# Kernel optimization log

Hardware: AMD Instinct MI355X
Metric: run time of the kernel (lower is better)

The kernel has to match this reference:

```python
import jax, jax.numpy as jnp
import numpy as np

N_Q_HEADS = 32
N_KV_HEADS = 8
GROUP = N_Q_HEADS // N_KV_HEADS  # 4


def _rope(x, cos, sin):
    # x: [b, s, h, d]; cos/sin: [s, d//2]. Complex rotation on (even, odd) pairs,
    # matching torch.view_as_complex on reshape(..., -1, 2).
    b, s, h, d = x.shape
    xr = x.reshape(b, s, h, d // 2, 2)
    x0, x1 = xr[..., 0], xr[..., 1]
    c = cos[None, :, None, :]
    sn = sin[None, :, None, :]
    o0 = x0 * c - x1 * sn
    o1 = x0 * sn + x1 * c
    return jnp.stack([o0, o1], axis=-1).reshape(b, s, h, d)


def setup_inputs() -> dict:
    key = jax.random.key(0)
    B, S, D = 2, 2048, 4096
    HD = D // N_Q_HEADS  # 128
    ks = jax.random.split(key, 8)
    x = jax.random.normal(ks[0], (B, S, D), jnp.float32)
    # True rotary table (theta = 10000), as cos/sin of shape [S, HD//2]
    inv_freq = 1.0 / (10000.0 ** (jnp.arange(0, HD, 2, dtype=jnp.float32) / HD))
    ang = jnp.outer(jnp.arange(S, dtype=jnp.float32), inv_freq)
    freqs_cos = jnp.cos(ang)
    freqs_sin = jnp.sin(ang)
    sc = 0.02
    qw = jax.random.normal(ks[1], (D, N_Q_HEADS * HD), jnp.float32) * sc
    qb = jax.random.normal(ks[2], (N_Q_HEADS * HD,), jnp.float32) * sc
    kw = jax.random.normal(ks[3], (D, N_KV_HEADS * HD), jnp.float32) * sc
    kb = jax.random.normal(ks[4], (N_KV_HEADS * HD,), jnp.float32) * sc
    vw = jax.random.normal(ks[5], (D, N_KV_HEADS * HD), jnp.float32) * sc
    vb = jax.random.normal(ks[6], (N_KV_HEADS * HD,), jnp.float32) * sc
    ow = jax.random.normal(ks[7], (D, D), jnp.float32) * sc
    return dict(x=x, freqs_cos=freqs_cos, freqs_sin=freqs_sin,
                qw=qw, qb=qb, kw=kw, kb=kb, vw=vw, vb=vb, ow=ow, start_pos=0)


def reference(x, freqs_cos, freqs_sin, qw, qb, kw, kb, vw, vb, ow, start_pos):
    b, s, dim = x.shape
    hd = dim // N_Q_HEADS
    q = (x @ qw + qb).reshape(b, s, N_Q_HEADS, hd)
    k = (x @ kw + kb).reshape(b, s, N_KV_HEADS, hd)
    v = (x @ vw + vb).reshape(b, s, N_KV_HEADS, hd)
    cos = freqs_cos[start_pos:start_pos + s]
    sin = freqs_sin[start_pos:start_pos + s]
    q = _rope(q, cos, sin)
    k = _rope(k, cos, sin)
    # start_pos == 0: cache write then slice is identity on fresh k/v.
    # GQA: query head h = kv_head * GROUP + g (matches torch repeat+reshape).
    q = q.transpose(0, 2, 1, 3).reshape(b, N_KV_HEADS, GROUP, s, hd)
    k = k.transpose(0, 2, 1, 3)  # [b, Hkv, s, hd]
    v = v.transpose(0, 2, 1, 3)
    scores = jnp.einsum('bhgqd,bhkd->bhgqk', q, k) / jnp.sqrt(jnp.float32(hd))
    causal = jnp.tril(jnp.ones((s, s), bool))
    scores = jnp.where(causal[None, None, None], scores, jnp.float32(-1e30))
    p = jax.nn.softmax(scores, axis=-1)
    o = jnp.einsum('bhgqk,bhkd->bhgqd', p, v)
    o = o.reshape(b, N_Q_HEADS, s, hd).transpose(0, 2, 1, 3).reshape(b, s, dim)
    return o @ ow
```

## Files before the change

kernel.cpp:

```cpp
#include <hip/hip_runtime.h>
#include <hip/hip_bf16.h>
#include <stdint.h>

typedef __bf16 bf16_t;
typedef __bf16 bf16x8 __attribute__((ext_vector_type(8)));
typedef __bf16 bf16x4 __attribute__((ext_vector_type(4)));
typedef float f32x4 __attribute__((ext_vector_type(4)));

typedef __attribute__((address_space(1))) unsigned gu32;
typedef __attribute__((address_space(3))) unsigned lu32;

__device__ __forceinline__ unsigned short f2bf(float f) {
  unsigned u = __builtin_bit_cast(unsigned, f);
  unsigned r = (u + 0x7FFFu + ((u >> 16) & 1u)) >> 16;
  return (unsigned short)r;
}

__device__ __forceinline__ void gload_lds16(const bf16_t* g, bf16_t* l) {
  __builtin_amdgcn_global_load_lds((const gu32*)(const void*)g, (lu32*)(void*)l, 16, 0, 0);
}

__global__ __launch_bounds__(256) void k_cvt_bf16(const float* __restrict__ in,
                                                  bf16_t* __restrict__ out, int n4) {
  int i = blockIdx.x * 256 + threadIdx.x;
  if (i >= n4) return;
  float4 v = ((const float4*)in)[i];
  ushort4 o;
  o.x = f2bf(v.x); o.y = f2bf(v.y); o.z = f2bf(v.z); o.w = f2bf(v.w);
  ((ushort4*)out)[i] = o;
}

__global__ __launch_bounds__(256) void k_transpose_cvt(const float* __restrict__ in,
                                                       bf16_t* __restrict__ out, int R, int C) {
  __shared__ float t[32][33];
  int c0 = blockIdx.x * 32, r0 = blockIdx.y * 32;
  int tx = threadIdx.x & 31, ty = threadIdx.x >> 5;
  #pragma unroll
  for (int r = 0; r < 4; ++r) {
    int rr = ty + r * 8;
    t[rr][tx] = in[(size_t)(r0 + rr) * C + c0 + tx];
  }
  __syncthreads();
  #pragma unroll
  for (int r = 0; r < 4; ++r) {
    int rr = ty + r * 8;
    ((unsigned short*)out)[(size_t)(c0 + rr) * R + r0 + tx] = f2bf(t[tx][rr]);
  }
}

__global__ __launch_bounds__(256) void k_transpose_bf16(const bf16_t* __restrict__ in,
                                                        bf16_t* __restrict__ out, int R, int C) {
  __shared__ unsigned short t[32][33];
  const unsigned short* ip = (const unsigned short*)in + (size_t)blockIdx.z * R * C;
  unsigned short* op = (unsigned short*)out + (size_t)blockIdx.z * R * C;
  int c0 = blockIdx.x * 32, r0 = blockIdx.y * 32;
  int tx = threadIdx.x & 31, ty = threadIdx.x >> 5;
  #pragma unroll
  for (int r = 0; r < 4; ++r) {
    int rr = ty + r * 8;
    t[rr][tx] = ip[(size_t)(r0 + rr) * C + c0 + tx];
  }
  __syncthreads();
  #pragma unroll
  for (int r = 0; r < 4; ++r) {
    int rr = ty + r * 8;
    op[(size_t)(c0 + rr) * R + r0 + tx] = t[tx][rr];
  }
}

#define BK 32
__global__ __launch_bounds__(256) void k_gemm_qkv(
    const bf16_t* __restrict__ A, const bf16_t* __restrict__ Bm,
    const float* __restrict__ qb, const float* __restrict__ kb, const float* __restrict__ vb,
    const float* __restrict__ cosT, const float* __restrict__ sinT,
    const int* __restrict__ start_pos,
    bf16_t* __restrict__ Qr, bf16_t* __restrict__ Kr, bf16_t* __restrict__ Vr) {
  __shared__ __attribute__((aligned(16))) bf16_t sA[128 * BK];
  __shared__ __attribute__((aligned(16))) bf16_t sB[128 * BK];
  __shared__ __attribute__((aligned(16))) bf16_t sET[128][132];
  const int tid = threadIdx.x;
  const int lane = tid & 63;
  const int wv = tid >> 6;
  const int wr = wv >> 1, wc = wv & 1;
  const int bid = blockIdx.y * gridDim.x + blockIdx.x;
  const int swz = (bid & 7) * 192 + (bid >> 3);
  const int brow = (swz & 31) * 128;
  const int bcol = (swz >> 5) * 128;
  const int K = 4096;
  const int l4 = lane >> 2;
  const int c8 = (lane & 3) * 8;
  const int fr = lane & 15;
  const int fq = lane >> 4;

  f32x4 acc[4][4];
  #pragma unroll
  for (int i = 0; i < 4; ++i)
    #pragma unroll
    for (int j = 0; j < 4; ++j) acc[i][j] = (f32x4){0.f, 0.f, 0.f, 0.f};

  for (int k0 = 0; k0 < K; k0 += BK) {
    #pragma unroll
    for (int r = 0; r < 2; ++r) {
      int chunk = r * 4 + wv;
      int row = chunk * 16 + l4;
      gload_lds16(A + (size_t)(brow + row) * K + k0 + c8, sA + chunk * 512);
      gload_lds16(Bm + (size_t)(bcol + row) * K + k0 + c8, sB + chunk * 512);
    }
    __syncthreads();
    bf16x8 af[4], bfv[4];
    #pragma unroll
    for (int mi = 0; mi < 4; ++mi)
      af[mi] = *(const bf16x8*)(sA + (wr * 64 + mi * 16 + fr) * BK + fq * 8);
    #pragma unroll
    for (int ni = 0; ni < 4; ++ni)
      bfv[ni] = *(const bf16x8*)(sB + (wc * 64 + ni * 16 + fr) * BK + fq * 8);
    #pragma unroll
    for (int mi = 0; mi < 4; ++mi)
      #pragma unroll
      for (int ni = 0; ni < 4; ++ni)
        acc[mi][ni] = __builtin_amdgcn_mfma_f32_16x16x32_bf16(af[mi], bfv[ni], acc[mi][ni], 0, 0, 0);
    __syncthreads();
  }

  const int sp = *start_pos;
  const bool isQ = bcol < 4096;
  const bool isV = bcol >= 5120;
  const int s0 = brow & 2047;
  #pragma unroll
  for (int mi = 0; mi < 4; ++mi) {
    #pragma unroll
    for (int ni = 0; ni < 4; ++ni) {
      int lc = wc * 64 + ni * 16 + fr;
      float bias = isQ ? qb[bcol + lc] : (!isV ? kb[bcol - 4096 + lc] : vb[bcol - 5120 + lc]);
      int lrb = wr * 64 + mi * 16 + fq * 4;
      bf16x4 pk;
      #pragma unroll
      for (int j = 0; j < 4; ++j) {
        float v = acc[mi][ni][j] + bias;
        float partner = __shfl_xor(v, 1);
        if (!isV) {
          int dd = lc >> 1;
          int s = s0 + lrb + j;
          float cc = cosT[(size_t)(sp + s) * 64 + dd];
          float sn = sinT[(size_t)(sp + s) * 64 + dd];
          v = (lc & 1) ? (partner * sn + v * cc) : (v * cc - partner * sn);
        }
        pk[j] = (bf16_t)v;
      }
      *(bf16x4*)&sET[lc][lrb] = pk;
    }
  }
  __syncthreads();
  const int b = brow >> 11;
  unsigned short* dst;
  if (isQ)
    dst = (unsigned short*)Qr + (((size_t)b * 32 + (bcol >> 7)) * 2048 + s0) * 128;
  else if (!isV)
    dst = (unsigned short*)Kr + (((size_t)b * 8 + ((bcol - 4096) >> 7)) * 2048 + s0) * 128;
  else
    dst = (unsigned short*)Vr + (((size_t)b * 8 + ((bcol - 5120) >> 7)) * 2048 + s0) * 128;
  #pragma unroll
  for (int i = 0; i < 8; ++i) {
    int chunk = i * 256 + tid;
    int sl = chunk >> 4;
    int dp = (chunk & 15) * 8;
    unsigned short tmp[8];
    #pragma unroll
    for (int k = 0; k < 8; ++k) tmp[k] = ((unsigned short*)sET)[(dp + k) * 132 + sl];
    uint4 ov;
    ov.x = (unsigned)tmp[0] | ((unsigned)tmp[1] << 16);
    ov.y = (unsigned)tmp[2] | ((unsigned)tmp[3] << 16);
    ov.z = (unsigned)tmp[4] | ((unsigned)tmp[5] << 16);
    ov.w = (unsigned)tmp[6] | ((unsigned)tmp[7] << 16);
    *(uint4*)(dst + (size_t)sl * 128 + dp) = ov;
  }
}

__global__ __launch_bounds__(256) void k_attn(
    const bf16_t* __restrict__ Qr, const bf16_t* __restrict__ Kr,
    const bf16_t* __restrict__ Vt, bf16_t* __restrict__ Ob) {
  __shared__ __attribute__((aligned(16))) bf16_t sK[2][4096];
  __shared__ __attribute__((aligned(16))) bf16_t sV[2][4096];
  __shared__ __attribute__((aligned(16))) bf16_t p_lds[4][16][40];

  const int tid = threadIdx.x;
  const int lane = tid & 63;
  const int w = tid >> 6;
  const int b = blockIdx.y >> 5, h = blockIdx.y & 31;
  const int hk = h >> 2;
  const int qt = (int)gridDim.x - 1 - (int)blockIdx.x;
  const int q0b = qt * 128;
  const int T = qt * 4 + 4;
  const bf16_t* Qb = Qr + (((size_t)b * 32 + h) * 2048) * 128;
  const bf16_t* Kb = Kr + (((size_t)b * 8 + hk) * 2048) * 128;
  const bf16_t* Vb = Vt + (((size_t)b * 8 + hk) * 128) * 2048;
  const int fr = lane & 15, fq = lane >> 4;
  const int qw0 = q0b + w * 32;
  const float sc = 0.08838834764831845f;

  const int c0 = w * 64 + lane;
  const int c1 = 256 + w * 64 + lane;
  const int krow0 = c0 >> 4, krow1 = c1 >> 4;
  const int ko0 = ((c0 & 15) << 4) ^ ((krow0 & 7) << 4);
  const int ko1 = ((c1 & 15) << 4) ^ ((krow1 & 7) << 4);
  const size_t ksrc0 = (size_t)krow0 * 128 + (ko0 >> 1);
  const size_t ksrc1 = (size_t)krow1 * 128 + (ko1 >> 1);
  const int vr0 = c0 >> 3, vr1 = c1 >> 3;
  const int vo0 = ((c0 & 7) << 4) ^ ((vr0 & 7) << 4);
  const int vo1 = ((c1 & 7) << 4) ^ ((vr1 & 7) << 4);
  const size_t vsrc0 = (size_t)(2 * vr0 + (vo0 >> 6)) * 2048 + ((vo0 & 63) >> 1);
  const size_t vsrc1 = (size_t)(2 * vr1 + (vo1 >> 6)) * 2048 + ((vo1 & 63) >> 1);
  const int ldsA = (w * 64) * 8;
  const int ldsB = (256 + w * 64) * 8;

  bf16x8 qf[2][4];
  #pragma unroll
  for (int f = 0; f < 2; ++f)
    #pragma unroll
    for (int c = 0; c < 4; ++c)
      qf[f][c] = *(const bf16x8*)(Qb + (size_t)(qw0 + f * 16 + fr) * 128 + c * 32 + fq * 8);

  f32x4 o[2][8];
  #pragma unroll
  for (int f = 0; f < 2; ++f)
    #pragma unroll
    for (int i = 0; i < 8; ++i) o[f][i] = (f32x4){0.f, 0.f, 0.f, 0.f};
  float m_s[2] = {-1e30f, -1e30f}, l_s[2] = {0.f, 0.f};

  const int kswz = (fr & 7) << 4;
  const int vlane = (fr >> 1) * 128 + ((((fr & 1) << 6) | (fq << 4)) ^ ((fr >> 1) << 4));

  auto STAGE = [&](int buf, int kv0) {
    const bf16_t* Kt = Kb + (size_t)kv0 * 128;
    const bf16_t* Vg = Vb + kv0;
    bf16_t* sk = &sK[buf][0];
    bf16_t* sv = &sV[buf][0];
    gload_lds16(Kt + ksrc0, sk + ldsA);
    gload_lds16(Kt + ksrc1, sk + ldsB);
    gload_lds16(Vg + vsrc0, sv + ldsA);
    gload_lds16(Vg + vsrc1, sv + ldsB);
  };

  STAGE(0, 0);
  int cur = 0;
  for (int t = 0; t < T; ++t) {
    const int kv0 = t * 32;
    if (t + 1 < T) {
      STAGE(cur ^ 1, kv0 + 32);
      asm volatile("s_waitcnt vmcnt(4)" ::: "memory");
    } else {
      asm volatile("s_waitcnt vmcnt(0)" ::: "memory");
    }
    __builtin_amdgcn_s_barrier();

    if (kv0 <= qw0 + 31) {
      const char* skc = (const char*)&sK[cur][0];
      const char* svc = (const char*)&sV[cur][0];
      f32x4 st[2][2];
      #pragma unroll
      for (int f = 0; f < 2; ++f)
        #pragma unroll
        for (int s2 = 0; s2 < 2; ++s2) st[f][s2] = (f32x4){0.f, 0.f, 0.f, 0.f};
      __builtin_amdgcn_s_setprio(1);
      #pragma unroll
      for (int c = 0; c < 4; ++c) {
        const int off = (((c << 6) | (fq << 4)) ^ kswz);
        bf16x8 kf0 = *(const bf16x8*)(skc + fr * 256 + off);
        bf16x8 kf1 = *(const bf16x8*)(skc + 4096 + fr * 256 + off);
        st[0][0] = __builtin_amdgcn_mfma_f32_16x16x32_bf16(kf0, qf[0][c], st[0][0], 0, 0, 0);
        st[0][1] = __builtin_amdgcn_mfma_f32_16x16x32_bf16(kf1, qf[0][c], st[0][1], 0, 0, 0);
        st[1][0] = __builtin_amdgcn_mfma_f32_16x16x32_bf16(kf0, qf[1][c], st[1][0], 0, 0, 0);
        st[1][1] = __builtin_amdgcn_mfma_f32_16x16x32_bf16(kf1, qf[1][c], st[1][1], 0, 0, 0);
      }
      __builtin_amdgcn_s_setprio(0);
      bf16x8 pa[2];
      #pragma unroll
      for (int f = 0; f < 2; ++f) {
        const int qg = qw0 + f * 16 + fr;
        float p0[4], p1[4];
        float pm = -1e30f;
        #pragma unroll
        for (int j = 0; j < 4; ++j) {
          int kvr = kv0 + fq * 4 + j;
          float s0v = (kvr <= qg) ? st[f][0][j] * sc : -1e30f;
          float s1v = (kvr + 16 <= qg) ? st[f][1][j] * sc : -1e30f;
          p0[j] = s0v; p1[j] = s1v;
          pm = fmaxf(pm, fmaxf(s0v, s1v));
        }
        pm = fmaxf(pm, __shfl_xor(pm, 16));
        pm = fmaxf(pm, __shfl_xor(pm, 32));
        if (!__all(pm <= m_s[f] + 8.0f)) {
          float m_new = fmaxf(m_s[f], pm);
          float scf = __expf(m_s[f] - m_new);
          l_s[f] *= scf;
          #pragma unroll
          for (int j = 0; j < 4; ++j) {
            float sj = __shfl(scf, fq * 4 + j);
            #pragma unroll
            for (int df = 0; df < 8; ++df) o[f][df][j] *= sj;
          }
          m_s[f] = m_new;
        }
        float ps = 0.f;
        #pragma unroll
        for (int j = 0; j < 4; ++j) {
          p0[j] = __expf(p0[j] - m_s[f]);
          p1[j] = __expf(p1[j] - m_s[f]);
          ps += p0[j] + p1[j];
        }
        ps += __shfl_xor(ps, 16);
        ps += __shfl_xor(ps, 32);
        l_s[f] += ps;
        bf16x4 pk0, pk1;
        #pragma unroll
        for (int j = 0; j < 4; ++j) { pk0[j] = (bf16_t)p0[j]; pk1[j] = (bf16_t)p1[j]; }
        *(bf16x4*)&p_lds[w][fr][fq * 4] = pk0;
        *(bf16x4*)&p_lds[w][fr][16 + fq * 4] = pk1;
        asm volatile("s_waitcnt lgkmcnt(0)" ::: "memory");
        pa[f] = *(const bf16x8*)&p_lds[w][fr][fq * 8];
        asm volatile("s_waitcnt lgkmcnt(0)" ::: "memory");
      }
      __builtin_amdgcn_s_setprio(1);
      #pragma unroll
      for (int df = 0; df < 8; ++df) {
        bf16x8 vf = *(const bf16x8*)(svc + df * 1024 + vlane);
        o[0][df] = __builtin_amdgcn_mfma_f32_16x16x32_bf16(pa[0], vf, o[0][df], 0, 0, 0);
        o[1][df] = __builtin_amdgcn_mfma_f32_16x16x32_bf16(pa[1], vf, o[1][df], 0, 0, 0);
      }
      __builtin_amdgcn_s_setprio(0);
    }
    __builtin_amdgcn_sched_barrier(0);
    __builtin_amdgcn_s_barrier();
    cur ^= 1;
  }

  #pragma unroll
  for (int f = 0; f < 2; ++f) {
    #pragma unroll
    for (int j = 0; j < 4; ++j) {
      float lj = __shfl(l_s[f], fq * 4 + j);
      float rl = 1.f / lj;
      int srow = qw0 + f * 16 + fq * 4 + j;
      #pragma unroll
      for (int df = 0; df < 8; ++df) {
        int dcol = df * 16 + fr;
        ((unsigned short*)Ob)[((size_t)b * 2048 + srow) * 4096 + h * 128 + dcol] =
            f2bf(o[f][df][j] * rl);
      }
    }
  }
}

__global__ __launch_bounds__(256) void k_gemm_out(
    const bf16_t* __restrict__ A, const bf16_t* __restrict__ Bm, float* __restrict__ out) {
  __shared__ __attribute__((aligned(16))) bf16_t sA[128 * BK];
  __shared__ __attribute__((aligned(16))) bf16_t sB[128 * BK];
  const int tid = threadIdx.x;
  const int lane = tid & 63;
  const int wv = tid >> 6;
  const int wr = wv >> 1, wc = wv & 1;
  const int bid = blockIdx.y * gridDim.x + blockIdx.x;
  const int swz = (bid & 7) * 128 + (bid >> 3);
  const int brow = (swz & 31) * 128;
  const int bcol = (swz >> 5) * 128;
  const int K = 4096;
  const int l4 = lane >> 2;
  const int c8 = (lane & 3) * 8;
  const int fr = lane & 15;
  const int fq = lane >> 4;

  f32x4 acc[4][4];
  #pragma unroll
  for (int i = 0; i < 4; ++i)
    #pragma unroll
    for (int j = 0; j < 4; ++j) acc[i][j] = (f32x4){0.f, 0.f, 0.f, 0.f};

  for (int k0 = 0; k0 < K; k0 += BK) {
    #pragma unroll
    for (int r = 0; r < 2; ++r) {
      int chunk = r * 4 + wv;
      int row = chunk * 16 + l4;
      gload_lds16(A + (size_t)(brow + row) * K + k0 + c8, sA + chunk * 512);
      gload_lds16(Bm + (size_t)(bcol + row) * K + k0 + c8, sB + chunk * 512);
    }
    __syncthreads();
    bf16x8 af[4], bfv[4];
    #pragma unroll
    for (int mi = 0; mi < 4; ++mi)
      af[mi] = *(const bf16x8*)(sA + (wr * 64 + mi * 16 + fr) * BK + fq * 8);
    #pragma unroll
    for (int ni = 0; ni < 4; ++ni)
      bfv[ni] = *(const bf16x8*)(sB + (wc * 64 + ni * 16 + fr) * BK + fq * 8);
    #pragma unroll
    for (int mi = 0; mi < 4; ++mi)
      #pragma unroll
      for (int ni = 0; ni < 4; ++ni)
        acc[mi][ni] = __builtin_amdgcn_mfma_f32_16x16x32_bf16(af[mi], bfv[ni], acc[mi][ni], 0, 0, 0);
    __syncthreads();
  }

  #pragma unroll
  for (int mi = 0; mi < 4; ++mi)
    #pragma unroll
    for (int ni = 0; ni < 4; ++ni) {
      int col = bcol + wc * 64 + ni * 16 + fr;
      #pragma unroll
      for (int j = 0; j < 4; ++j) {
        int row = brow + wr * 64 + mi * 16 + fq * 4 + j;
        out[(size_t)row * 4096 + col] = acc[mi][ni][j];
      }
    }
}

extern "C" void kernel_launch(void* const* d_in, const int* in_sizes, int n_in,
                              void* d_out, int out_size, void* d_ws, size_t ws_size,
                              hipStream_t stream) {
  const float* x    = (const float*)d_in[0];
  const float* cosT = (const float*)d_in[1];
  const float* sinT = (const float*)d_in[2];
  const float* qw   = (const float*)d_in[3];
  const float* qb   = (const float*)d_in[4];
  const float* kw   = (const float*)d_in[5];
  const float* kb   = (const float*)d_in[6];
  const float* vw   = (const float*)d_in[7];
  const float* vb   = (const float*)d_in[8];
  const float* ow   = (const float*)d_in[9];
  const int*   sp   = (const int*)d_in[10];
  float* out = (float*)d_out;
  char* ws = (char*)d_ws;

  bf16_t* xb  = (bf16_t*)(ws + 0);
  bf16_t* Ob  = (bf16_t*)(ws + 0);
  bf16_t* wT  = (bf16_t*)(ws + (size_t)33554432);
  bf16_t* owT = (bf16_t*)(ws + (size_t)83886080);
  bf16_t* Qr  = (bf16_t*)(ws + (size_t)117440512);
  bf16_t* Kr  = (bf16_t*)(ws + (size_t)150994944);
  bf16_t* Vr  = (bf16_t*)(ws + (size_t)159383552);
  bf16_t* Vt  = (bf16_t*)(ws + (size_t)167772160);

  k_cvt_bf16<<<16384, 256, 0, stream>>>(x, xb, 2 * 2048 * 4096 / 4);
  k_transpose_cvt<<<dim3(128, 128), 256, 0, stream>>>(qw, wT, 4096, 4096);
  k_transpose_cvt<<<dim3(32, 128), 256, 0, stream>>>(kw, wT + (size_t)4096 * 4096, 4096, 1024);
  k_transpose_cvt<<<dim3(32, 128), 256, 0, stream>>>(vw, wT + (size_t)5120 * 4096, 4096, 1024);
  k_transpose_cvt<<<dim3(128, 128), 256, 0, stream>>>(ow, owT, 4096, 4096);

  k_gemm_qkv<<<dim3(32, 48), 256, 0, stream>>>(xb, wT, qb, kb, vb, cosT, sinT, sp, Qr, Kr, Vr);
  k_transpose_bf16<<<dim3(4, 64, 16), 256, 0, stream>>>(Vr, Vt, 2048, 128);
  k_attn<<<dim3(16, 64), 256, 0, stream>>>(Qr, Kr, Vt, Ob);
  k_gemm_out<<<dim3(32, 32), 256, 0, stream>>>(Ob, owT, out);
}
```

Baseline: 958.7 us.

## Replace both GEMMs with a pipelined 256x256-tile, 512-thread templated kernel

Merges the QKV and output projection GEMMs into one templated kernel. It uses 256x256 block tiles, 8 waves and double-buffered 128KB dynamic LDS with XOR-swizzled layouts. Global-to-LDS loads for the next K tile are interleaved with MFMA half-steps, paced by explicit vmcnt waits, raw barriers and s_setprio around MFMA bursts. This raises data reuse per loaded byte and hides load latency, at the cost of fewer blocks per CU and a partial last wave for the QKV grid (384 blocks). The RoPE/bias epilogue is run in two passes through an LDS transpose buffer.

```diff
diff --git a/kernel.cpp b/kernel.cpp
--- a/kernel.cpp
+++ b/kernel.cpp
@@ -19,6 +19,9 @@
 __device__ __forceinline__ void gload_lds16(const bf16_t* g, bf16_t* l) {
   __builtin_amdgcn_global_load_lds((const gu32*)(const void*)g, (lu32*)(void*)l, 16, 0, 0);
 }
+
+#define BARRIER() do { asm volatile("" ::: "memory"); __builtin_amdgcn_s_barrier(); asm volatile("" ::: "memory"); } while (0)
+#define WAITV(N) asm volatile("s_waitcnt vmcnt(" #N ")" ::: "memory")
 
 __global__ __launch_bounds__(256) void k_cvt_bf16(const float* __restrict__ in,
                                                   bf16_t* __restrict__ out, int n4) {
@@ -68,111 +71,167 @@
   }
 }
 
-#define BK 32
-__global__ __launch_bounds__(256) void k_gemm_qkv(
+template <int MODE>
+__global__ __launch_bounds__(512, 2) void k_gemm256(
     const bf16_t* __restrict__ A, const bf16_t* __restrict__ Bm,
     const float* __restrict__ qb, const float* __restrict__ kb, const float* __restrict__ vb,
     const float* __restrict__ cosT, const float* __restrict__ sinT,
     const int* __restrict__ start_pos,
-    bf16_t* __restrict__ Qr, bf16_t* __restrict__ Kr, bf16_t* __restrict__ Vr) {
-  __shared__ __attribute__((aligned(16))) bf16_t sA[128 * BK];
-  __shared__ __attribute__((aligned(16))) bf16_t sB[128 * BK];
-  __shared__ __attribute__((aligned(16))) bf16_t sET[128][132];
+    bf16_t* __restrict__ Qr, bf16_t* __restrict__ Kr, bf16_t* __restrict__ Vr,
+    float* __restrict__ outF, int nbq) {
+  extern __shared__ char smem[];
+  bf16_t* sAe = (bf16_t*)smem;
+  bf16_t* sBe = (bf16_t*)(smem + 65536);
   const int tid = threadIdx.x;
   const int lane = tid & 63;
-  const int wv = tid >> 6;
-  const int wr = wv >> 1, wc = wv & 1;
-  const int bid = blockIdx.y * gridDim.x + blockIdx.x;
-  const int swz = (bid & 7) * 192 + (bid >> 3);
-  const int brow = (swz & 31) * 128;
-  const int bcol = (swz >> 5) * 128;
-  const int K = 4096;
-  const int l4 = lane >> 2;
-  const int c8 = (lane & 3) * 8;
-  const int fr = lane & 15;
-  const int fq = lane >> 4;
-
-  f32x4 acc[4][4];
-  #pragma unroll
-  for (int i = 0; i < 4; ++i)
-    #pragma unroll
-    for (int j = 0; j < 4; ++j) acc[i][j] = (f32x4){0.f, 0.f, 0.f, 0.f};
-
-  for (int k0 = 0; k0 < K; k0 += BK) {
-    #pragma unroll
-    for (int r = 0; r < 2; ++r) {
-      int chunk = r * 4 + wv;
-      int row = chunk * 16 + l4;
-      gload_lds16(A + (size_t)(brow + row) * K + k0 + c8, sA + chunk * 512);
-      gload_lds16(Bm + (size_t)(bcol + row) * K + k0 + c8, sB + chunk * 512);
+  const int w = tid >> 6;
+  const int wr = w >> 2, wc = w & 3;
+  const int fr = lane & 15, fq = lane >> 4;
+  const int g = (blockIdx.x & 7) * nbq + (blockIdx.x >> 3);
+  const int brow = (g & 15) * 256;
+  const int bcol = (g >> 4) * 256;
+
+  const int srow = w * 16 + (lane >> 2);
+  const int scol = (((lane & 3) ^ ((lane >> 3) & 3))) * 8;
+  const bf16_t* Ag = A + (size_t)(brow + srow) * 4096 + scol;
+  const bf16_t* Bg = Bm + (size_t)(bcol + srow) * 4096 + scol;
+  bf16_t* sAw = sAe + w * 512;
+  bf16_t* sBw = sBe + w * 512;
+
+  const int swz = (fr >> 1) & 3;
+  const int aoff = (wr * 128 + fr) * 32 + (fq ^ swz) * 8;
+  const int boff = (wc * 64 + fr) * 32 + (fq ^ swz) * 8;
+
+  f32x4 acc[8][4];
+  #pragma unroll
+  for (int m = 0; m < 8; ++m)
+    #pragma unroll
+    for (int n = 0; n < 4; ++n) acc[m][n] = (f32x4){0.f, 0.f, 0.f, 0.f};
+
+  auto stageA = [&](int buf, int kh, int kt) {
+    const bf16_t* gp = Ag + (size_t)kt * 64 + kh * 32;
+    bf16_t* lp = sAw + (buf * 2 + kh) * 8192;
+    gload_lds16(gp, lp);
+    gload_lds16(gp + (size_t)128 * 4096, lp + 4096);
+  };
+  auto stageB = [&](int buf, int kh, int kt) {
+    const bf16_t* gp = Bg + (size_t)kt * 64 + kh * 32;
+    bf16_t* lp = sBw + (buf * 2 + kh) * 8192;
+    gload_lds16(gp, lp);
+    gload_lds16(gp + (size_t)128 * 4096, lp + 4096);
+  };
+
+  bf16x8 afv[4], bfv[4];
+#define LOADB(BUF, KH) { const bf16_t* p = sBe + ((BUF) * 2 + (KH)) * 8192 + boff; \
+  _Pragma("unroll") for (int n = 0; n < 4; ++n) bfv[n] = *(const bf16x8*)(p + n * 512); }
+#define LOADA(BUF, KH, MH) { const bf16_t* p = sAe + ((BUF) * 2 + (KH)) * 8192 + aoff + (MH) * 2048; \
+  _Pragma("unroll") for (int m = 0; m < 4; ++m) afv[m] = *(const bf16x8*)(p + m * 512); }
+#define MFMAH(MH) do { __builtin_amdgcn_s_setprio(1); \
+  _Pragma("unroll") for (int m = 0; m < 4; ++m) \
+    _Pragma("unroll") for (int n = 0; n < 4; ++n) \
+      acc[(MH) * 4 + m][n] = __builtin_amdgcn_mfma_f32_16x16x32_bf16(afv[m], bfv[n], acc[(MH) * 4 + m][n], 0, 0, 0); \
+  __builtin_amdgcn_s_setprio(0); } while (0)
+
+  stageA(0, 0, 0); stageB(0, 0, 0);
+  stageA(0, 1, 0); stageB(0, 1, 0);
+  WAITV(4);
+  BARRIER();
+
+  for (int kt = 0; kt < 63; ++kt) {
+    const int cur = kt & 1, nxt = cur ^ 1;
+    LOADB(cur, 0); LOADA(cur, 0, 0); stageA(nxt, 0, kt + 1);
+    BARRIER(); MFMAH(0); BARRIER();
+    LOADA(cur, 0, 1); stageB(nxt, 0, kt + 1);
+    BARRIER(); MFMAH(1); WAITV(4); BARRIER();
+    LOADB(cur, 1); LOADA(cur, 1, 0); stageA(nxt, 1, kt + 1);
+    BARRIER(); MFMAH(0); BARRIER();
+    LOADA(cur, 1, 1); stageB(nxt, 1, kt + 1);
+    BARRIER(); MFMAH(1); WAITV(4); BARRIER();
+  }
+  LOADB(1, 0); LOADA(1, 0, 0); BARRIER(); MFMAH(0); BARRIER();
+  LOADA(1, 0, 1); BARRIER(); MFMAH(1); WAITV(0); BARRIER();
+  LOADB(1, 1); LOADA(1, 1, 0); BARRIER(); MFMAH(0); BARRIER();
+  LOADA(1, 1, 1); MFMAH(1);
+#undef LOADB
+#undef LOADA
+#undef MFMAH
+
+  __syncthreads();
+
+  if constexpr (MODE == 0) {
+    const int sp2 = *start_pos;
+    const int b = brow >> 11;
+    const int s0 = brow & 2047;
+    const bool isV = (bcol >= 5120);
+    unsigned short* sET = (unsigned short*)smem;
+    const int hh = wc >> 1;
+    const int dbase = (wc & 1) * 64;
+    #pragma unroll
+    for (int pass = 0; pass < 2; ++pass) {
+      if (hh == pass) {
+        #pragma unroll
+        for (int n = 0; n < 4; ++n) {
+          const int d = dbase + n * 16 + fr;
+          const int col = bcol + pass * 128 + d;
+          float bias;
+          if (bcol < 4096) bias = qb[col];
+          else if (bcol < 5120) bias = kb[col - 4096];
+          else bias = vb[col - 5120];
+          #pragma unroll
+          for (int m = 0; m < 8; ++m) {
+            const int sl = wr * 128 + m * 16 + fq * 4;
+            bf16x4 pk;
+            #pragma unroll
+            for (int j = 0; j < 4; ++j) {
+              float v = acc[m][n][j] + bias;
+              float partner = __shfl_xor(v, 1);
+              if (!isV) {
+                int s = s0 + sl + j;
+                float cc = cosT[(size_t)(sp2 + s) * 64 + (d >> 1)];
+                float sn = sinT[(size_t)(sp2 + s) * 64 + (d >> 1)];
+                v = (d & 1) ? (partner * sn + v * cc) : (v * cc - partner * sn);
+              }
+              pk[j] = (bf16_t)v;
+            }
+            *(bf16x4*)&sET[d * 268 + sl] = pk;
+          }
+        }
+      }
+      __syncthreads();
+      const int cb = bcol + pass * 128;
+      unsigned short* Hdst;
+      if (cb < 4096)      Hdst = (unsigned short*)Qr + (((size_t)b * 32 + (cb >> 7)) * 2048 + s0) * 128;
+      else if (cb < 5120) Hdst = (unsigned short*)Kr + (((size_t)b * 8 + ((cb - 4096) >> 7)) * 2048 + s0) * 128;
+      else                Hdst = (unsigned short*)Vr + (((size_t)b * 8 + ((cb - 5120) >> 7)) * 2048 + s0) * 128;
+      #pragma unroll
+      for (int i = 0; i < 8; ++i) {
+        int c = i * 512 + tid;
+        int sl = c >> 4;
+        int dp = (c & 15) * 8;
+        unsigned short tmp[8];
+        #pragma unroll
+        for (int k2 = 0; k2 < 8; ++k2) tmp[k2] = sET[(dp + k2) * 268 + sl];
+        uint4 ov;
+        ov.x = (unsigned)tmp[0] | ((unsigned)tmp[1] << 16);
+        ov.y = (unsigned)tmp[2] | ((unsigned)tmp[3] << 16);
+        ov.z = (unsigned)tmp[4] | ((unsigned)tmp[5] << 16);
+        ov.w = (unsigned)tmp[6] | ((unsigned)tmp[7] << 16);
+        *(uint4*)(Hdst + (size_t)sl * 128 + dp) = ov;
+      }
+      __syncthreads();
     }
-    __syncthreads();
-    bf16x8 af[4], bfv[4];
-    #pragma unroll
-    for (int mi = 0; mi < 4; ++mi)
-      af[mi] = *(const bf16x8*)(sA + (wr * 64 + mi * 16 + fr) * BK + fq * 8);
-    #pragma unroll
-    for (int ni = 0; ni < 4; ++ni)
-      bfv[ni] = *(const bf16x8*)(sB + (wc * 64 + ni * 16 + fr) * BK + fq * 8);
-    #pragma unroll
-    for (int mi = 0; mi < 4; ++mi)
-      #pragma unroll
-      for (int ni = 0; ni < 4; ++ni)
-        acc[mi][ni] = __builtin_amdgcn_mfma_f32_16x16x32_bf16(af[mi], bfv[ni], acc[mi][ni], 0, 0, 0);
-    __syncthreads();
-  }
-
-  const int sp = *start_pos;
-  const bool isQ = bcol < 4096;
-  const bool isV = bcol >= 5120;
-  const int s0 = brow & 2047;
-  #pragma unroll
-  for (int mi = 0; mi < 4; ++mi) {
-    #pragma unroll
-    for (int ni = 0; ni < 4; ++ni) {
-      int lc = wc * 64 + ni * 16 + fr;
-      float bias = isQ ? qb[bcol + lc] : (!isV ? kb[bcol - 4096 + lc] : vb[bcol - 5120 + lc]);
-      int lrb = wr * 64 + mi * 16 + fq * 4;
-      bf16x4 pk;
-      #pragma unroll
-      for (int j = 0; j < 4; ++j) {
-        float v = acc[mi][ni][j] + bias;
-        float partner = __shfl_xor(v, 1);
-        if (!isV) {
-          int dd = lc >> 1;
-          int s = s0 + lrb + j;
-          float cc = cosT[(size_t)(sp + s) * 64 + dd];
-          float sn = sinT[(size_t)(sp + s) * 64 + dd];
-          v = (lc & 1) ? (partner * sn + v * cc) : (v * cc - partner * sn);
+  } else {
+    #pragma unroll
+    for (int m = 0; m < 8; ++m)
+      #pragma unroll
+      for (int n = 0; n < 4; ++n) {
+        const int col = bcol + wc * 64 + n * 16 + fr;
+        #pragma unroll
+        for (int j = 0; j < 4; ++j) {
+          const int row = brow + wr * 128 + m * 16 + fq * 4 + j;
+          outF[(size_t)row * 4096 + col] = acc[m][n][j];
         }
-        pk[j] = (bf16_t)v;
-      }
-      *(bf16x4*)&sET[lc][lrb] = pk;
-    }
-  }
-  __syncthreads();
-  const int b = brow >> 11;
-  unsigned short* dst;
-  if (isQ)
-    dst = (unsigned short*)Qr + (((size_t)b * 32 + (bcol >> 7)) * 2048 + s0) * 128;
-  else if (!isV)
-    dst = (unsigned short*)Kr + (((size_t)b * 8 + ((bcol - 4096) >> 7)) * 2048 + s0) * 128;
-  else
-    dst = (unsigned short*)Vr + (((size_t)b * 8 + ((bcol - 5120) >> 7)) * 2048 + s0) * 128;
-  #pragma unroll
-  for (int i = 0; i < 8; ++i) {
-    int chunk = i * 256 + tid;
-    int sl = chunk >> 4;
-    int dp = (chunk & 15) * 8;
-    unsigned short tmp[8];
-    #pragma unroll
-    for (int k = 0; k < 8; ++k) tmp[k] = ((unsigned short*)sET)[(dp + k) * 132 + sl];
-    uint4 ov;
-    ov.x = (unsigned)tmp[0] | ((unsigned)tmp[1] << 16);
-    ov.y = (unsigned)tmp[2] | ((unsigned)tmp[3] << 16);
-    ov.z = (unsigned)tmp[4] | ((unsigned)tmp[5] << 16);
-    ov.w = (unsigned)tmp[6] | ((unsigned)tmp[7] << 16);
-    *(uint4*)(dst + (size_t)sl * 128 + dp) = ov;
+      }
   }
 }
 
@@ -351,67 +410,6 @@
   }
 }
 
-__global__ __launch_bounds__(256) void k_gemm_out(
-    const bf16_t* __restrict__ A, const bf16_t* __restrict__ Bm, float* __restrict__ out) {
-  __shared__ __attribute__((aligned(16))) bf16_t sA[128 * BK];
-  __shared__ __attribute__((aligned(16))) bf16_t sB[128 * BK];
-  const int tid = threadIdx.x;
-  const int lane = tid & 63;
-  const int wv = tid >> 6;
-  const int wr = wv >> 1, wc = wv & 1;
-  const int bid = blockIdx.y * gridDim.x + blockIdx.x;
-  const int swz = (bid & 7) * 128 + (bid >> 3);
-  const int brow = (swz & 31) * 128;
-  const int bcol = (swz >> 5) * 128;
-  const int K = 4096;
-  const int l4 = lane >> 2;
-  const int c8 = (lane & 3) * 8;
-  const int fr = lane & 15;
-  const int fq = lane >> 4;
-
-  f32x4 acc[4][4];
-  #pragma unroll
-  for (int i = 0; i < 4; ++i)
-    #pragma unroll
-    for (int j = 0; j < 4; ++j) acc[i][j] = (f32x4){0.f, 0.f, 0.f, 0.f};
-
-  for (int k0 = 0; k0 < K; k0 += BK) {
-    #pragma unroll
-    for (int r = 0; r < 2; ++r) {
-      int chunk = r * 4 + wv;
-      int row = chunk * 16 + l4;
-      gload_lds16(A + (size_t)(brow + row) * K + k0 + c8, sA + chunk * 512);
-      gload_lds16(Bm + (size_t)(bcol + row) * K + k0 + c8, sB + chunk * 512);
-    }
-    __syncthreads();
-    bf16x8 af[4], bfv[4];
-    #pragma unroll
-    for (int mi = 0; mi < 4; ++mi)
-      af[mi] = *(const bf16x8*)(sA + (wr * 64 + mi * 16 + fr) * BK + fq * 8);
-    #pragma unroll
-    for (int ni = 0; ni < 4; ++ni)
-      bfv[ni] = *(const bf16x8*)(sB + (wc * 64 + ni * 16 + fr) * BK + fq * 8);
-    #pragma unroll
-    for (int mi = 0; mi < 4; ++mi)
-      #pragma unroll
-      for (int ni = 0; ni < 4; ++ni)
-        acc[mi][ni] = __builtin_amdgcn_mfma_f32_16x16x32_bf16(af[mi], bfv[ni], acc[mi][ni], 0, 0, 0);
-    __syncthreads();
-  }
-
-  #pragma unroll
-  for (int mi = 0; mi < 4; ++mi)
-    #pragma unroll
-    for (int ni = 0; ni < 4; ++ni) {
-      int col = bcol + wc * 64 + ni * 16 + fr;
-      #pragma unroll
-      for (int j = 0; j < 4; ++j) {
-        int row = brow + wr * 64 + mi * 16 + fq * 4 + j;
-        out[(size_t)row * 4096 + col] = acc[mi][ni][j];
-      }
-    }
-}
-
 extern "C" void kernel_launch(void* const* d_in, const int* in_sizes, int n_in,
                               void* d_out, int out_size, void* d_ws, size_t ws_size,
                               hipStream_t stream) {
@@ -438,14 +436,19 @@
   bf16_t* Vr  = (bf16_t*)(ws + (size_t)159383552);
   bf16_t* Vt  = (bf16_t*)(ws + (size_t)167772160);
 
+  const int shmem = 131072;
+  hipFuncSetAttribute((const void*)&k_gemm256<0>, hipFuncAttributeMaxDynamicSharedMemorySize, shmem);
+  hipFuncSetAttribute((const void*)&k_gemm256<1>, hipFuncAttributeMaxDynamicSharedMemorySize, shmem);
+
   k_cvt_bf16<<<16384, 256, 0, stream>>>(x, xb, 2 * 2048 * 4096 / 4);
   k_transpose_cvt<<<dim3(128, 128), 256, 0, stream>>>(qw, wT, 4096, 4096);
   k_transpose_cvt<<<dim3(32, 128), 256, 0, stream>>>(kw, wT + (size_t)4096 * 4096, 4096, 1024);
   k_transpose_cvt<<<dim3(32, 128), 256, 0, stream>>>(vw, wT + (size_t)5120 * 4096, 4096, 1024);
   k_transpose_cvt<<<dim3(128, 128), 256, 0, stream>>>(ow, owT, 4096, 4096);
 
-  k_gemm_qkv<<<dim3(32, 48), 256, 0, stream>>>(xb, wT, qb, kb, vb, cosT, sinT, sp, Qr, Kr, Vr);
+  k_gemm256<0><<<384, 512, shmem, stream>>>(xb, wT, qb, kb, vb, cosT, sinT, sp, Qr, Kr, Vr, nullptr, 48);
   k_transpose_bf16<<<dim3(4, 64, 16), 256, 0, stream>>>(Vr, Vt, 2048, 128);
   k_attn<<<dim3(16, 64), 256, 0, stream>>>(Qr, Kr, Vt, Ob);
-  k_gemm_out<<<dim3(32, 32), 256, 0, stream>>>(Ob, owT, out);
-}
+  k_gemm256<1><<<256, 512, shmem, stream>>>(Ob, owT, nullptr, nullptr, nullptr, nullptr, nullptr, nullptr,
+                                            nullptr, nullptr, nullptr, out, 32);
+}
```

Result: faster. 920.5 us (-4.0%).
